# Kernel tuning notes

Measured on AMD Instinct MI355X. Metric: run time of the kernel, lower is better.

Reference implementation:

```python
import jax, jax.numpy as jnp
import numpy as np

D_MODEL = 1024

def setup_inputs() -> dict:
    key = jax.random.key(0)
    ks = jax.random.split(key, 5)
    s = 1.0 / np.sqrt(D_MODEL)  # torch Linear default init scale-ish
    x = jax.random.normal(ks[0], (4, 2048, D_MODEL), dtype=jnp.float32)
    Wq = jax.random.normal(ks[1], (D_MODEL, D_MODEL), dtype=jnp.float32) * s
    Wk = jax.random.normal(ks[2], (D_MODEL, D_MODEL), dtype=jnp.float32) * s
    Wv = jax.random.normal(ks[3], (D_MODEL, D_MODEL), dtype=jnp.float32) * s
    Wo = jax.random.normal(ks[4], (D_MODEL, D_MODEL), dtype=jnp.float32) * s
    z = jnp.zeros((D_MODEL,), dtype=jnp.float32)
    return {"x": x, "Wq": Wq, "bq": z, "Wk": Wk, "bk": z, "Wv": Wv, "bv": z, "Wo": Wo, "bo": z}

def reference(x, Wq, bq, Wk, bk, Wv, bv, Wo, bo):
    # x: (B, S, D). Single-head causal attention, dropout in eval mode (identity).
    B, S, D = x.shape
    Q = jnp.einsum('bsd,ed->bse', x, Wq) + bq
    K = jnp.einsum('bsd,ed->bse', x, Wk) + bk
    V = jnp.einsum('bsd,ed->bse', x, Wv) + bv
    scores = jnp.einsum('bqd,bkd->bqk', Q, K) / jnp.sqrt(jnp.float32(D))
    causal = jnp.tril(jnp.ones((S, S), dtype=bool))  # (S, S)
    scores = jnp.where(causal, scores, -jnp.inf)
    weights = jax.nn.softmax(scores, axis=-1)
    attended = jnp.einsum('bqk,bkd->bqd', weights, V)
    out = jnp.einsum('bsd,ed->bse', attended, Wo) + bo
    return out
```

## Files before the change

### kernel.cpp

```cpp
#include <hip/hip_runtime.h>
#include <cstdint>
#include <cstddef>


#define D_MODEL 1024
#define SEQ     2048
#define BATCH   4

typedef unsigned short u16;
typedef __bf16 bf16_t;
typedef bf16_t bf16x8 __attribute__((ext_vector_type(8)));
typedef float  f32x4  __attribute__((ext_vector_type(4)));
typedef u16    u16x4  __attribute__((ext_vector_type(4)));

__device__ __forceinline__ u16 f2bf(float x) {
  union { float f; uint32_t u; } v; v.f = x;
  uint32_t r = v.u + 0x7fffu + ((v.u >> 16) & 1u);
  return (u16)(r >> 16);
}

__device__ __forceinline__ void gload_lds16(const u16* g, u16* l) {
  __builtin_amdgcn_global_load_lds((__attribute__((address_space(1))) void*)g,
                                   (__attribute__((address_space(3))) void*)l,
                                   16, 0, 0);
}

template <bool ROWSUM>
__device__ __forceinline__ void gemm_core(const u16* __restrict__ A,
                                          const u16* __restrict__ B,
                                          int lda, int ldb, int nt,
                                          u16* As, u16* Bs,
                                          f32x4 acc[4][4], f32x4* rs) {
  const int tid  = threadIdx.x;
  const int lane = tid & 63, wave = tid >> 6;
  const int frow = lane & 15, kc = lane >> 4;
  const int abase = (wave >> 2) * 64, bbase = (wave & 3) * 64;
  const int ar = tid >> 2;
  const int ac = (tid & 3) ^ ((ar >> 1) & 3);
  const u16* Asrc  = A + (size_t)ar * lda + ac * 8;
  const u16* Bsrc0 = B + (size_t)ar * ldb + ac * 8;
  const u16* Bsrc1 = B + (size_t)(ar + 128) * ldb + ac * 8;
  int aoff[4], boff[4];
#pragma unroll
  for (int i = 0; i < 4; ++i) {
    const int ra = abase + i * 16 + frow;
    aoff[i] = (ra * 4 + (kc ^ ((ra >> 1) & 3))) * 8;
    const int rb = bbase + i * 16 + frow;
    boff[i] = (rb * 4 + (kc ^ ((rb >> 1) & 3))) * 8;
  }
  bf16x8 ones;
  if (ROWSUM) {
#pragma unroll
    for (int r = 0; r < 8; ++r) ((u16*)&ones)[r] = 0x3F80;
  }
  auto stage = [&](int t) {
    u16* ab = As + (t & 3) * 4096;
    u16* bb = Bs + (t & 3) * 8192;
    const int kb = t * 32;
    gload_lds16(Asrc + kb, ab + tid * 8);
    gload_lds16(Bsrc0 + kb, bb + tid * 8);
    gload_lds16(Bsrc1 + kb, bb + 4096 + tid * 8);
  };
  stage(0);
  if (nt > 1) stage(1);
  if (nt > 2) stage(2);
  for (int t = 0; t < nt; ++t) {
    if (t + 2 < nt)      asm volatile("s_waitcnt vmcnt(6)" ::: "memory");
    else if (t + 1 < nt) asm volatile("s_waitcnt vmcnt(3)" ::: "memory");
    else                 asm volatile("s_waitcnt vmcnt(0)" ::: "memory");
    __builtin_amdgcn_s_barrier();
    asm volatile("" ::: "memory");
    const u16* ab = As + (t & 3) * 4096;
    const u16* bb = Bs + (t & 3) * 8192;
    bf16x8 af[4], bf[4];
#pragma unroll
    for (int j = 0; j < 4; ++j) bf[j] = *(const bf16x8*)(bb + boff[j]);
#pragma unroll
    for (int i = 0; i < 4; ++i) af[i] = *(const bf16x8*)(ab + aoff[i]);
    if (t + 3 < nt) stage(t + 3);
    __builtin_amdgcn_s_setprio(1);
#pragma unroll
    for (int i = 0; i < 4; ++i)
#pragma unroll
      for (int j = 0; j < 4; ++j)
        acc[i][j] = __builtin_amdgcn_mfma_f32_16x16x32_bf16(af[i], bf[j], acc[i][j], 0, 0, 0);
    if (ROWSUM) {
#pragma unroll
      for (int i = 0; i < 4; ++i)
        rs[i] = __builtin_amdgcn_mfma_f32_16x16x32_bf16(af[i], ones, rs[i], 0, 0, 0);
    }
    __builtin_amdgcn_s_setprio(0);
    asm volatile("" ::: "memory");
    __builtin_amdgcn_s_barrier();
  }
}

__global__ __launch_bounds__(256) void cvt_kernel(const float4* __restrict__ x,
                                                  const float4* __restrict__ wq,
                                                  const float4* __restrict__ wk,
                                                  const float4* __restrict__ wv,
                                                  const float4* __restrict__ wo,
                                                  u16* __restrict__ dst) {
  const int i = blockIdx.x * 256 + threadIdx.x;
  float4 v;
  if (i < 2097152) {
    v = x[i];
  } else {
    const int j = i - 2097152;
    const int w = j >> 18;
    const float4* s = (w == 0) ? wq : (w == 1) ? wk : (w == 2) ? wv : wo;
    v = s[j & 262143];
  }
  u16x4 o = {f2bf(v.x), f2bf(v.y), f2bf(v.z), f2bf(v.w)};
  *(u16x4*)(dst + (size_t)i * 4) = o;
}

__global__ void transposeW_kernel(const u16* __restrict__ src, u16* __restrict__ dst) {
  __shared__ u16 tile[32][33];
  const int r0 = blockIdx.x * 32, c0 = blockIdx.y * 32;
  const int tx = threadIdx.x, ty = threadIdx.y;
#pragma unroll
  for (int r = 0; r < 4; ++r)
    tile[ty + r * 8][tx] = src[(size_t)(r0 + ty + r * 8) * D_MODEL + c0 + tx];
  __syncthreads();
#pragma unroll
  for (int r = 0; r < 4; ++r)
    dst[(size_t)(c0 + ty + r * 8) * D_MODEL + r0 + tx] = tile[tx][ty + r * 8];
}

__global__ __launch_bounds__(512, 2) void stageA_kernel(
    const u16* __restrict__ xb,
    const u16* __restrict__ WqB, const u16* __restrict__ WkB,
    const u16* __restrict__ WoB, const u16* __restrict__ WvT,
    const float* __restrict__ Wo32, const float* __restrict__ bv,
    const float* __restrict__ bq, const float* __restrict__ bk,
    u16* __restrict__ Qb, u16* __restrict__ Kb,
    u16* __restrict__ Wp, float* __restrict__ bp) {
  __shared__ __align__(16) u16 As[16384];
  __shared__ __align__(16) u16 Bs[32768];
  const int blk = blockIdx.x, tid = threadIdx.x;
  const int lane = tid & 63, wave = tid >> 6;
  const int abase = (wave >> 2) * 64, bbase = (wave & 3) * 64;
  const int cl = lane & 15, rl = (lane >> 4) * 4;
  const int c = blk & 7, i = blk >> 3;

  {
    const int rt   = c * 8 + (i & 7);
    const int czi  = i >> 3;
    const int row0 = rt * 128, col0 = (czi >> 1) * 256, z = czi & 1;
    const u16*   W    = z ? WkB : WqB;
    const float* bias = z ? bk : bq;
    u16*         out  = z ? Kb : Qb;
    f32x4 acc[4][4] = {};
    gemm_core<false>(xb + (size_t)row0 * D_MODEL, W + (size_t)col0 * D_MODEL,
                     D_MODEL, D_MODEL, 32, As, Bs, acc, nullptr);
#pragma unroll
    for (int j = 0; j < 4; ++j) {
      const int col = col0 + bbase + j * 16 + cl;
      const float bb = bias[col];
#pragma unroll
      for (int ii = 0; ii < 4; ++ii)
#pragma unroll
        for (int r = 0; r < 4; ++r) {
          const int row = row0 + abase + ii * 16 + rl + r;
          out[(size_t)row * D_MODEL + col] = f2bf(acc[ii][j][r] + bb);
        }
    }
  }
  if (i < 4) {
    const int widx = c * 4 + i;
    const int f0 = (widx >> 2) * 128, e0 = (widx & 3) * 256;
    f32x4 acc[4][4] = {};
    gemm_core<false>(WoB + (size_t)f0 * D_MODEL, WvT + (size_t)e0 * D_MODEL,
                     D_MODEL, D_MODEL, 32, As, Bs, acc, nullptr);
#pragma unroll
    for (int j = 0; j < 4; ++j) {
      const int col = e0 + bbase + j * 16 + cl;
#pragma unroll
      for (int ii = 0; ii < 4; ++ii)
#pragma unroll
        for (int r = 0; r < 4; ++r) {
          const int row = f0 + abase + ii * 16 + rl + r;
          Wp[(size_t)row * D_MODEL + col] = f2bf(acc[ii][j][r]);
        }
    }
  } else if (i < 6) {
    const int f  = (c * 2 + (i - 4)) * 64 + (tid >> 3);
    const int dq = tid & 7;
    const float* row = Wo32 + (size_t)f * D_MODEL + dq * 128;
    const float* bvq = bv + dq * 128;
    float s = 0.f;
#pragma unroll 8
    for (int k = 0; k < 128; ++k) s += row[k] * bvq[k];
    s += __shfl_xor(s, 1);
    s += __shfl_xor(s, 2);
    s += __shfl_xor(s, 4);
    if (dq == 0) bp[f] = s;
  }
}

__global__ __launch_bounds__(512, 2) void stageB_kernel(
    const u16* __restrict__ xb, const u16* __restrict__ Wp,
    const float* __restrict__ bp,
    const u16* __restrict__ Qb, const u16* __restrict__ Kb,
    u16* __restrict__ Vt, u16* __restrict__ Eb) {
  __shared__ __align__(16) u16 As[16384];
  __shared__ __align__(16) u16 Bs[32768];
  const int blk = blockIdx.x, tid = threadIdx.x;
  const int lane = tid & 63, wave = tid >> 6;
  const int abase = (wave >> 2) * 64, bbase = (wave & 3) * 64;
  const int cl = lane & 15, rl = (lane >> 4) * 4;

  if (blk < 256) {
    const int c = blk & 7;
    const int nunit = (blk < 224) ? 1 : 2;
    int uid = (blk < 224) ? (blk >> 3) : (28 + ((blk - 224) >> 3) * 2);
    for (int uu = 0; uu < nunit; ++uu, ++uid) {
      const int w = c * 36 + uid;
      const int b = w / 72;
      int r = w % 72, qi = 0;
#pragma unroll 1
      for (; qi < 16; ++qi) { const int n = (qi >> 1) + 1; if (r < n) break; r -= n; }
      const int ji = r;
      const u16* A  = Qb + (size_t)(b * SEQ + qi * 128) * D_MODEL;
      const u16* Bt = Kb + (size_t)(b * SEQ + ji * 256) * D_MODEL;
      f32x4 acc[4][4] = {};
      gemm_core<false>(A, Bt, D_MODEL, D_MODEL, 32, As, Bs, acc, nullptr);
      u16* out = Eb + (size_t)b * SEQ * SEQ;
#pragma unroll
      for (int ii = 0; ii < 4; ++ii)
#pragma unroll
        for (int rr = 0; rr < 4; ++rr) {
          const int q = qi * 128 + abase + ii * 16 + rl + rr;
#pragma unroll
          for (int j = 0; j < 4; ++j) {
            const int jj = ji * 256 + bbase + j * 16 + cl;
            out[(size_t)q * SEQ + jj] =
                (jj <= q) ? f2bf(__expf(acc[ii][j][rr] * 0.03125f)) : (u16)0;
          }
        }
    }
  } else {
    const int v = blk - 256;
    const int c = v & 7, s = v >> 3;
    const int row0 = (c * 8 + (s >> 2)) * 128;
    const int col0 = (s & 3) * 256;
    f32x4 acc[4][4] = {};
    gemm_core<false>(xb + (size_t)row0 * D_MODEL, Wp + (size_t)col0 * D_MODEL,
                     D_MODEL, D_MODEL, 32, As, Bs, acc, nullptr);
    const int b = row0 >> 11;
    u16* vt = Vt + (size_t)b * D_MODEL * SEQ;
#pragma unroll
    for (int j = 0; j < 4; ++j) {
      const int col = col0 + bbase + j * 16 + cl;
      const float bb = bp[col];
#pragma unroll
      for (int ii = 0; ii < 4; ++ii) {
        const int s0 = (row0 & 2047) + abase + ii * 16 + rl;
        u16x4 o = {f2bf(acc[ii][j][0] + bb), f2bf(acc[ii][j][1] + bb),
                   f2bf(acc[ii][j][2] + bb), f2bf(acc[ii][j][3] + bb)};
        *(u16x4*)(vt + (size_t)col * SEQ + s0) = o;
      }
    }
  }
}

__global__ __launch_bounds__(512, 2) void pv_kernel(const u16* __restrict__ Eb,
                                                    const u16* __restrict__ Vt,
                                                    const float* __restrict__ bo,
                                                    float* __restrict__ Out) {
  __shared__ __align__(16) u16 As[16384];
  __shared__ __align__(16) u16 Bs[32768];
  const int blk = blockIdx.x, tid = threadIdx.x;
  const int c = blk & 7, i = blk >> 3;
  const int b  = c >> 1;
  const int dt = (c & 1) * 2 + (i >> 4);
  const int qt = i & 15;
  const u16* A  = Eb + (size_t)b * SEQ * SEQ + (size_t)(qt * 128) * SEQ;
  const u16* Bt = Vt + (size_t)b * D_MODEL * SEQ + (size_t)(dt * 256) * SEQ;
  f32x4 acc[4][4] = {};
  f32x4 rs[4] = {};
  gemm_core<true>(A, Bt, SEQ, SEQ, (qt + 1) * 4, As, Bs, acc, rs);
  const int lane = tid & 63, wave = tid >> 6;
  const int abase = (wave >> 2) * 64, bbase = (wave & 3) * 64;
  const int cl = lane & 15, rl = (lane >> 4) * 4;
#pragma unroll
  for (int ii = 0; ii < 4; ++ii)
#pragma unroll
    for (int r = 0; r < 4; ++r) {
      const float invl = 1.0f / rs[ii][r];
      const int row = b * SEQ + qt * 128 + abase + ii * 16 + rl + r;
#pragma unroll
      for (int j = 0; j < 4; ++j) {
        const int col = dt * 256 + bbase + j * 16 + cl;
        Out[(size_t)row * D_MODEL + col] = acc[ii][j][r] * invl + bo[col];
      }
    }
}

extern "C" void kernel_launch(void* const* d_in, const int* in_sizes, int n_in,
                              void* d_out, int out_size, void* d_ws, size_t ws_size,
                              hipStream_t stream) {
  const float* x  = (const float*)d_in[0];
  const float* Wq = (const float*)d_in[1];
  const float* bq = (const float*)d_in[2];
  const float* Wk = (const float*)d_in[3];
  const float* bk = (const float*)d_in[4];
  const float* Wv = (const float*)d_in[5];
  const float* bv = (const float*)d_in[6];
  const float* Wo = (const float*)d_in[7];
  const float* bo = (const float*)d_in[8];
  float* out = (float*)d_out;
  char* ws = (char*)d_ws;

  u16*   xb  = (u16*)(ws);
  u16*   Wb  = (u16*)(ws + (16u << 20));
  u16*   Qb  = (u16*)(ws + (24u << 20));
  u16*   Kb  = (u16*)(ws + (40u << 20));
  u16*   Vt  = (u16*)(ws + (56u << 20));
  u16*   Eb  = (u16*)(ws + (72u << 20));
  u16*   WvT = (u16*)(ws + (104u << 20));
  u16*   Wp  = (u16*)(ws + (106u << 20));
  float* bp  = (float*)(ws + (108u << 20));

  cvt_kernel<<<12288, 256, 0, stream>>>((const float4*)x, (const float4*)Wq,
                                        (const float4*)Wk, (const float4*)Wv,
                                        (const float4*)Wo, xb);
  transposeW_kernel<<<dim3(32, 32), dim3(32, 8), 0, stream>>>(Wb + (2u << 20), WvT);
  stageA_kernel<<<512, 512, 0, stream>>>(xb, Wb, Wb + (1u << 20), Wb + (3u << 20),
                                         WvT, Wo, bv, bq, bk, Qb, Kb, Wp, bp);
  stageB_kernel<<<512, 512, 0, stream>>>(xb, Wp, bp, Qb, Kb, Vt, Eb);
  pv_kernel<<<256, 512, 0, stream>>>(Eb, Vt, bo, out);
}
```

Baseline: 258.1 us.

## Retile GEMMs to 256x256, move softmax rowsum into score epilogue, rebalance PV

The QK/QKV projection and score GEMMs now use a 256x256 block tile with a triple-buffered LDS pipeline and one barrier per k-step, which raises arithmetic intensity per block. Causal score tiles are remapped to 256-row blocks with a hand-balanced schedule. The softmax row sums are computed in the score epilogue from the bf16-rounded exponentials and accumulated with atomics into a zeroed workspace buffer, so the extra rowsum MFMAs in the PV kernel go away. The PV kernel switches to 128x128 tiles with short and long causal rows paired for load balance and higher occupancy. The cost is atomic traffic, an extra memset launch, and a risk of tail imbalance from the uneven tile mix.

```diff
diff --git a/kernel.cpp b/kernel.cpp
--- a/kernel.cpp
+++ b/kernel.cpp
@@ -18,6 +18,10 @@
   uint32_t r = v.u + 0x7fffu + ((v.u >> 16) & 1u);
   return (u16)(r >> 16);
 }
+__device__ __forceinline__ float bf2f(u16 h) {
+  union { uint32_t u; float f; } v; v.u = (uint32_t)h << 16;
+  return v.f;
+}
 
 __device__ __forceinline__ void gload_lds16(const u16* g, u16* l) {
   __builtin_amdgcn_global_load_lds((__attribute__((address_space(1))) void*)g,
@@ -25,73 +29,126 @@
                                    16, 0, 0);
 }
 
-template <bool ROWSUM>
-__device__ __forceinline__ void gemm_core(const u16* __restrict__ A,
-                                          const u16* __restrict__ B,
-                                          int lda, int ldb, int nt,
-                                          u16* As, u16* Bs,
-                                          f32x4 acc[4][4], f32x4* rs) {
+__device__ __forceinline__ void gemm256(const u16* __restrict__ A,
+                                        const u16* __restrict__ B,
+                                        int lda, int ldb, int nt,
+                                        u16* As, u16* Bs,
+                                        f32x4 acc[8][4]) {
   const int tid  = threadIdx.x;
   const int lane = tid & 63, wave = tid >> 6;
   const int frow = lane & 15, kc = lane >> 4;
-  const int abase = (wave >> 2) * 64, bbase = (wave & 3) * 64;
-  const int ar = tid >> 2;
-  const int ac = (tid & 3) ^ ((ar >> 1) & 3);
-  const u16* Asrc  = A + (size_t)ar * lda + ac * 8;
-  const u16* Bsrc0 = B + (size_t)ar * ldb + ac * 8;
-  const u16* Bsrc1 = B + (size_t)(ar + 128) * ldb + ac * 8;
-  int aoff[4], boff[4];
+  const int abase = (wave >> 2) * 128, bbase = (wave & 3) * 64;
+  const int r0 = tid >> 2;
+  const int k0 = ((tid & 3) ^ ((r0 >> 1) & 3)) * 8;
+  const u16* Asrc0 = A + (size_t)r0 * lda + k0;
+  const u16* Asrc1 = A + (size_t)(r0 + 128) * lda + k0;
+  const u16* Bsrc0 = B + (size_t)r0 * ldb + k0;
+  const u16* Bsrc1 = B + (size_t)(r0 + 128) * ldb + k0;
+  int aoff[8], boff[4];
+#pragma unroll
+  for (int i = 0; i < 8; ++i) {
+    const int ra = abase + i * 16 + frow;
+    aoff[i] = (ra * 4 + (kc ^ ((ra >> 1) & 3))) * 8;
+  }
+#pragma unroll
+  for (int j = 0; j < 4; ++j) {
+    const int rb = bbase + j * 16 + frow;
+    boff[j] = (rb * 4 + (kc ^ ((rb >> 1) & 3))) * 8;
+  }
+  auto stage = [&](int t, int bufi) {
+    u16* ab = As + bufi * 8192;
+    u16* bb = Bs + bufi * 8192;
+    const int kb = t * 32;
+    gload_lds16(Asrc0 + kb, ab + tid * 8);
+    gload_lds16(Asrc1 + kb, ab + 4096 + tid * 8);
+    gload_lds16(Bsrc0 + kb, bb + tid * 8);
+    gload_lds16(Bsrc1 + kb, bb + 4096 + tid * 8);
+  };
+  stage(0, 0);
+  if (nt > 1) stage(1, 1);
+  int cb = 0, sb = 2;
+  for (int t = 0; t < nt; ++t) {
+    if (t + 1 < nt) asm volatile("s_waitcnt vmcnt(4)" ::: "memory");
+    else            asm volatile("s_waitcnt vmcnt(0)" ::: "memory");
+    __builtin_amdgcn_s_barrier();
+    asm volatile("" ::: "memory");
+    if (t + 2 < nt) stage(t + 2, sb);
+    const u16* ab = As + cb * 8192;
+    const u16* bb = Bs + cb * 8192;
+    bf16x8 af[8], bf[4];
+#pragma unroll
+    for (int j = 0; j < 4; ++j) bf[j] = *(const bf16x8*)(bb + boff[j]);
+#pragma unroll
+    for (int i = 0; i < 8; ++i) af[i] = *(const bf16x8*)(ab + aoff[i]);
+    __builtin_amdgcn_s_setprio(1);
+#pragma unroll
+    for (int i = 0; i < 8; ++i)
+#pragma unroll
+      for (int j = 0; j < 4; ++j)
+        acc[i][j] = __builtin_amdgcn_mfma_f32_16x16x32_bf16(af[i], bf[j], acc[i][j], 0, 0, 0);
+    __builtin_amdgcn_s_setprio(0);
+    asm volatile("" ::: "memory");
+    cb = (cb == 2) ? 0 : cb + 1;
+    sb = (sb == 2) ? 0 : sb + 1;
+  }
+}
+
+__device__ __forceinline__ void gemm128(const u16* __restrict__ A,
+                                        const u16* __restrict__ B,
+                                        int lda, int ldb, int nt,
+                                        u16* As, u16* Bs,
+                                        f32x4 acc[4][2]) {
+  const int tid  = threadIdx.x;
+  const int lane = tid & 63, wave = tid >> 6;
+  const int frow = lane & 15, kc = lane >> 4;
+  const int abase = (wave >> 2) * 64, bbase = (wave & 3) * 32;
+  const int r0 = tid >> 2;
+  const int k0 = ((tid & 3) ^ ((r0 >> 1) & 3)) * 8;
+  const u16* Asrc = A + (size_t)r0 * lda + k0;
+  const u16* Bsrc = B + (size_t)r0 * ldb + k0;
+  int aoff[4], boff[2];
 #pragma unroll
   for (int i = 0; i < 4; ++i) {
     const int ra = abase + i * 16 + frow;
     aoff[i] = (ra * 4 + (kc ^ ((ra >> 1) & 3))) * 8;
-    const int rb = bbase + i * 16 + frow;
-    boff[i] = (rb * 4 + (kc ^ ((rb >> 1) & 3))) * 8;
-  }
-  bf16x8 ones;
-  if (ROWSUM) {
-#pragma unroll
-    for (int r = 0; r < 8; ++r) ((u16*)&ones)[r] = 0x3F80;
+  }
+#pragma unroll
+  for (int j = 0; j < 2; ++j) {
+    const int rb = bbase + j * 16 + frow;
+    boff[j] = (rb * 4 + (kc ^ ((rb >> 1) & 3))) * 8;
   }
   auto stage = [&](int t) {
     u16* ab = As + (t & 3) * 4096;
-    u16* bb = Bs + (t & 3) * 8192;
+    u16* bb = Bs + (t & 3) * 4096;
     const int kb = t * 32;
     gload_lds16(Asrc + kb, ab + tid * 8);
-    gload_lds16(Bsrc0 + kb, bb + tid * 8);
-    gload_lds16(Bsrc1 + kb, bb + 4096 + tid * 8);
+    gload_lds16(Bsrc + kb, bb + tid * 8);
   };
   stage(0);
   if (nt > 1) stage(1);
   if (nt > 2) stage(2);
   for (int t = 0; t < nt; ++t) {
-    if (t + 2 < nt)      asm volatile("s_waitcnt vmcnt(6)" ::: "memory");
-    else if (t + 1 < nt) asm volatile("s_waitcnt vmcnt(3)" ::: "memory");
+    if (t + 2 < nt)      asm volatile("s_waitcnt vmcnt(4)" ::: "memory");
+    else if (t + 1 < nt) asm volatile("s_waitcnt vmcnt(2)" ::: "memory");
     else                 asm volatile("s_waitcnt vmcnt(0)" ::: "memory");
     __builtin_amdgcn_s_barrier();
     asm volatile("" ::: "memory");
+    if (t + 3 < nt) stage(t + 3);
     const u16* ab = As + (t & 3) * 4096;
-    const u16* bb = Bs + (t & 3) * 8192;
-    bf16x8 af[4], bf[4];
-#pragma unroll
-    for (int j = 0; j < 4; ++j) bf[j] = *(const bf16x8*)(bb + boff[j]);
+    const u16* bb = Bs + (t & 3) * 4096;
+    bf16x8 af[4], bf[2];
+#pragma unroll
+    for (int j = 0; j < 2; ++j) bf[j] = *(const bf16x8*)(bb + boff[j]);
 #pragma unroll
     for (int i = 0; i < 4; ++i) af[i] = *(const bf16x8*)(ab + aoff[i]);
-    if (t + 3 < nt) stage(t + 3);
     __builtin_amdgcn_s_setprio(1);
 #pragma unroll
     for (int i = 0; i < 4; ++i)
 #pragma unroll
-      for (int j = 0; j < 4; ++j)
+      for (int j = 0; j < 2; ++j)
         acc[i][j] = __builtin_amdgcn_mfma_f32_16x16x32_bf16(af[i], bf[j], acc[i][j], 0, 0, 0);
-    if (ROWSUM) {
-#pragma unroll
-      for (int i = 0; i < 4; ++i)
-        rs[i] = __builtin_amdgcn_mfma_f32_16x16x32_bf16(af[i], ones, rs[i], 0, 0, 0);
-    }
     __builtin_amdgcn_s_setprio(0);
     asm volatile("" ::: "memory");
-    __builtin_amdgcn_s_barrier();
   }
 }
 
@@ -136,45 +193,47 @@
     const float* __restrict__ bq, const float* __restrict__ bk,
     u16* __restrict__ Qb, u16* __restrict__ Kb,
     u16* __restrict__ Wp, float* __restrict__ bp) {
-  __shared__ __align__(16) u16 As[16384];
-  __shared__ __align__(16) u16 Bs[32768];
+  __shared__ __align__(16) u16 As[24576];
+  __shared__ __align__(16) u16 Bs[24576];
   const int blk = blockIdx.x, tid = threadIdx.x;
   const int lane = tid & 63, wave = tid >> 6;
-  const int abase = (wave >> 2) * 64, bbase = (wave & 3) * 64;
   const int cl = lane & 15, rl = (lane >> 4) * 4;
-  const int c = blk & 7, i = blk >> 3;
-
-  {
-    const int rt   = c * 8 + (i & 7);
-    const int czi  = i >> 3;
-    const int row0 = rt * 128, col0 = (czi >> 1) * 256, z = czi & 1;
+
+  if (blk < 256) {
+    const int c = blk & 7, i = blk >> 3;
+    const int z = i >> 4, w = i & 15;
+    const int rt = c * 4 + (w >> 2), ct = w & 3;
+    const int row0 = rt * 256, col0 = ct * 256;
     const u16*   W    = z ? WkB : WqB;
     const float* bias = z ? bk : bq;
     u16*         out  = z ? Kb : Qb;
-    f32x4 acc[4][4] = {};
-    gemm_core<false>(xb + (size_t)row0 * D_MODEL, W + (size_t)col0 * D_MODEL,
-                     D_MODEL, D_MODEL, 32, As, Bs, acc, nullptr);
+    f32x4 acc[8][4] = {};
+    gemm256(xb + (size_t)row0 * D_MODEL, W + (size_t)col0 * D_MODEL,
+            D_MODEL, D_MODEL, 32, As, Bs, acc);
+    const int abase = (wave >> 2) * 128, bbase = (wave & 3) * 64;
 #pragma unroll
     for (int j = 0; j < 4; ++j) {
       const int col = col0 + bbase + j * 16 + cl;
       const float bb = bias[col];
 #pragma unroll
-      for (int ii = 0; ii < 4; ++ii)
+      for (int ii = 0; ii < 8; ++ii)
 #pragma unroll
         for (int r = 0; r < 4; ++r) {
           const int row = row0 + abase + ii * 16 + rl + r;
           out[(size_t)row * D_MODEL + col] = f2bf(acc[ii][j][r] + bb);
         }
     }
-  }
-  if (i < 4) {
-    const int widx = c * 4 + i;
-    const int f0 = (widx >> 2) * 128, e0 = (widx & 3) * 256;
-    f32x4 acc[4][4] = {};
-    gemm_core<false>(WoB + (size_t)f0 * D_MODEL, WvT + (size_t)e0 * D_MODEL,
-                     D_MODEL, D_MODEL, 32, As, Bs, acc, nullptr);
-#pragma unroll
-    for (int j = 0; j < 4; ++j) {
+  } else if (blk < 320) {
+    const int qq = blk - 256;
+    const int t16 = qq >> 2, quad = qq & 3;
+    const int f0 = (t16 >> 2) * 256 + (quad >> 1) * 128;
+    const int e0 = (t16 & 3) * 256 + (quad & 1) * 128;
+    f32x4 acc[4][2] = {};
+    gemm128(WoB + (size_t)f0 * D_MODEL, WvT + (size_t)e0 * D_MODEL,
+            D_MODEL, D_MODEL, 32, As, Bs, acc);
+    const int abase = (wave >> 2) * 64, bbase = (wave & 3) * 32;
+#pragma unroll
+    for (int j = 0; j < 2; ++j) {
       const int col = e0 + bbase + j * 16 + cl;
 #pragma unroll
       for (int ii = 0; ii < 4; ++ii)
@@ -184,8 +243,8 @@
           Wp[(size_t)row * D_MODEL + col] = f2bf(acc[ii][j][r]);
         }
     }
-  } else if (i < 6) {
-    const int f  = (c * 2 + (i - 4)) * 64 + (tid >> 3);
+  } else {
+    const int f  = (blk - 320) * 64 + (tid >> 3);
     const int dq = tid & 7;
     const float* row = Wo32 + (size_t)f * D_MODEL + dq * 128;
     const float* bvq = bv + dq * 128;
@@ -203,55 +262,91 @@
     const u16* __restrict__ xb, const u16* __restrict__ Wp,
     const float* __restrict__ bp,
     const u16* __restrict__ Qb, const u16* __restrict__ Kb,
-    u16* __restrict__ Vt, u16* __restrict__ Eb) {
-  __shared__ __align__(16) u16 As[16384];
-  __shared__ __align__(16) u16 Bs[32768];
+    u16* __restrict__ Vt, u16* __restrict__ Eb, float* __restrict__ rssum) {
+  __shared__ __align__(16) u16 As[24576];
+  __shared__ __align__(16) u16 Bs[24576];
   const int blk = blockIdx.x, tid = threadIdx.x;
   const int lane = tid & 63, wave = tid >> 6;
-  const int abase = (wave >> 2) * 64, bbase = (wave & 3) * 64;
   const int cl = lane & 15, rl = (lane >> 4) * 4;
 
-  if (blk < 256) {
-    const int c = blk & 7;
-    const int nunit = (blk < 224) ? 1 : 2;
-    int uid = (blk < 224) ? (blk >> 3) : (28 + ((blk - 224) >> 3) * 2);
-    for (int uu = 0; uu < nunit; ++uu, ++uid) {
-      const int w = c * 36 + uid;
-      const int b = w / 72;
-      int r = w % 72, qi = 0;
-#pragma unroll 1
-      for (; qi < 16; ++qi) { const int n = (qi >> 1) + 1; if (r < n) break; r -= n; }
-      const int ji = r;
-      const u16* A  = Qb + (size_t)(b * SEQ + qi * 128) * D_MODEL;
-      const u16* Bt = Kb + (size_t)(b * SEQ + ji * 256) * D_MODEL;
-      f32x4 acc[4][4] = {};
-      gemm_core<false>(A, Bt, D_MODEL, D_MODEL, 32, As, Bs, acc, nullptr);
-      u16* out = Eb + (size_t)b * SEQ * SEQ;
-#pragma unroll
-      for (int ii = 0; ii < 4; ++ii)
-#pragma unroll
-        for (int rr = 0; rr < 4; ++rr) {
-          const int q = qi * 128 + abase + ii * 16 + rl + rr;
-#pragma unroll
-          for (int j = 0; j < 4; ++j) {
-            const int jj = ji * 256 + bbase + j * 16 + cl;
-            out[(size_t)q * SEQ + jj] =
-                (jj <= q) ? f2bf(__expf(acc[ii][j][rr] * 0.03125f)) : (u16)0;
-          }
+  if (blk < 144) {
+    const int c = blk & 7, u = blk >> 3;
+    const int b = c >> 1, h = c & 1;
+    int qi, ji;
+    if (h == 0) {
+      if (u < 1)       { qi = 0; ji = u; }
+      else if (u < 5)  { qi = 3; ji = u - 1; }
+      else if (u < 10) { qi = 4; ji = u - 5; }
+      else             { qi = 7; ji = u - 10; }
+    } else {
+      if (u < 2)       { qi = 1; ji = u; }
+      else if (u < 5)  { qi = 2; ji = u - 2; }
+      else if (u < 11) { qi = 5; ji = u - 5; }
+      else             { qi = 6; ji = u - 11; }
+    }
+    const u16* A  = Qb + (size_t)(b * SEQ + qi * 256) * D_MODEL;
+    const u16* Bt = Kb + (size_t)(b * SEQ + ji * 256) * D_MODEL;
+    f32x4 acc[8][4] = {};
+    gemm256(A, Bt, D_MODEL, D_MODEL, 32, As, Bs, acc);
+    u16* outp = Eb + (size_t)b * SEQ * SEQ;
+    float* rs = rssum + b * SEQ;
+    const int abase = (wave >> 2) * 128, bbase = (wave & 3) * 64;
+#pragma unroll
+    for (int ii = 0; ii < 8; ++ii)
+#pragma unroll
+      for (int r = 0; r < 4; ++r) {
+        const int q = qi * 256 + abase + ii * 16 + rl + r;
+        float ps = 0.f;
+#pragma unroll
+        for (int j = 0; j < 4; ++j) {
+          const int jj = ji * 256 + bbase + j * 16 + cl;
+          u16 h16 = 0;
+          if (jj <= q) h16 = f2bf(__expf(acc[ii][j][r] * 0.03125f));
+          outp[(size_t)q * SEQ + jj] = h16;
+          ps += bf2f(h16);
         }
-    }
-  } else {
-    const int v = blk - 256;
-    const int c = v & 7, s = v >> 3;
-    const int row0 = (c * 8 + (s >> 2)) * 128;
-    const int col0 = (s & 3) * 256;
-    f32x4 acc[4][4] = {};
-    gemm_core<false>(xb + (size_t)row0 * D_MODEL, Wp + (size_t)col0 * D_MODEL,
-                     D_MODEL, D_MODEL, 32, As, Bs, acc, nullptr);
+        ps += __shfl_xor(ps, 1);
+        ps += __shfl_xor(ps, 2);
+        ps += __shfl_xor(ps, 4);
+        ps += __shfl_xor(ps, 8);
+        if (cl == 0) atomicAdd(&rs[q], ps);
+      }
+  } else if (blk < 256) {
+    const int v = blk - 144;
+    const int rt = v >> 2, ct = v & 3;
+    const int row0 = rt * 256, col0 = ct * 256;
+    f32x4 acc[8][4] = {};
+    gemm256(xb + (size_t)row0 * D_MODEL, Wp + (size_t)col0 * D_MODEL,
+            D_MODEL, D_MODEL, 32, As, Bs, acc);
     const int b = row0 >> 11;
     u16* vt = Vt + (size_t)b * D_MODEL * SEQ;
+    const int abase = (wave >> 2) * 128, bbase = (wave & 3) * 64;
 #pragma unroll
     for (int j = 0; j < 4; ++j) {
+      const int col = col0 + bbase + j * 16 + cl;
+      const float bb = bp[col];
+#pragma unroll
+      for (int ii = 0; ii < 8; ++ii) {
+        const int s0 = (row0 & 2047) + abase + ii * 16 + rl;
+        u16x4 o = {f2bf(acc[ii][j][0] + bb), f2bf(acc[ii][j][1] + bb),
+                   f2bf(acc[ii][j][2] + bb), f2bf(acc[ii][j][3] + bb)};
+        *(u16x4*)(vt + (size_t)col * SEQ + s0) = o;
+      }
+    }
+  } else {
+    const int qq = blk - 256;
+    const int t16 = qq >> 2, quad = qq & 3;
+    const int rt = 28 + (t16 >> 2), ct = t16 & 3;
+    const int row0 = rt * 256 + (quad >> 1) * 128;
+    const int col0 = ct * 256 + (quad & 1) * 128;
+    f32x4 acc[4][2] = {};
+    gemm128(xb + (size_t)row0 * D_MODEL, Wp + (size_t)col0 * D_MODEL,
+            D_MODEL, D_MODEL, 32, As, Bs, acc);
+    const int b = row0 >> 11;
+    u16* vt = Vt + (size_t)b * D_MODEL * SEQ;
+    const int abase = (wave >> 2) * 64, bbase = (wave & 3) * 32;
+#pragma unroll
+    for (int j = 0; j < 2; ++j) {
       const int col = col0 + bbase + j * 16 + cl;
       const float bb = bp[col];
 #pragma unroll
@@ -265,35 +360,35 @@
   }
 }
 
-__global__ __launch_bounds__(512, 2) void pv_kernel(const u16* __restrict__ Eb,
+__global__ __launch_bounds__(512, 4) void pv_kernel(const u16* __restrict__ Eb,
                                                     const u16* __restrict__ Vt,
+                                                    const float* __restrict__ rssum,
                                                     const float* __restrict__ bo,
                                                     float* __restrict__ Out) {
   __shared__ __align__(16) u16 As[16384];
-  __shared__ __align__(16) u16 Bs[32768];
+  __shared__ __align__(16) u16 Bs[16384];
   const int blk = blockIdx.x, tid = threadIdx.x;
-  const int c = blk & 7, i = blk >> 3;
-  const int b  = c >> 1;
-  const int dt = (c & 1) * 2 + (i >> 4);
-  const int qt = i & 15;
+  const int rr = blk >> 8, idx = blk & 255;
+  const int b = idx >> 6, rest = idx & 63;
+  const int dt8 = rest >> 3, m = rest & 7;
+  const int qt = rr ? (15 - 2 * m) : (2 * m);
   const u16* A  = Eb + (size_t)b * SEQ * SEQ + (size_t)(qt * 128) * SEQ;
-  const u16* Bt = Vt + (size_t)b * D_MODEL * SEQ + (size_t)(dt * 256) * SEQ;
-  f32x4 acc[4][4] = {};
-  f32x4 rs[4] = {};
-  gemm_core<true>(A, Bt, SEQ, SEQ, (qt + 1) * 4, As, Bs, acc, rs);
+  const u16* Bt = Vt + (size_t)b * D_MODEL * SEQ + (size_t)(dt8 * 128) * SEQ;
+  f32x4 acc[4][2] = {};
+  gemm128(A, Bt, SEQ, SEQ, (qt + 1) * 4, As, Bs, acc);
   const int lane = tid & 63, wave = tid >> 6;
-  const int abase = (wave >> 2) * 64, bbase = (wave & 3) * 64;
+  const int abase = (wave >> 2) * 64, bbase = (wave & 3) * 32;
   const int cl = lane & 15, rl = (lane >> 4) * 4;
 #pragma unroll
   for (int ii = 0; ii < 4; ++ii)
 #pragma unroll
     for (int r = 0; r < 4; ++r) {
-      const float invl = 1.0f / rs[ii][r];
-      const int row = b * SEQ + qt * 128 + abase + ii * 16 + rl + r;
-#pragma unroll
-      for (int j = 0; j < 4; ++j) {
-        const int col = dt * 256 + bbase + j * 16 + cl;
-        Out[(size_t)row * D_MODEL + col] = acc[ii][j][r] * invl + bo[col];
+      const int row = qt * 128 + abase + ii * 16 + rl + r;
+      const float invl = 1.0f / rssum[b * SEQ + row];
+#pragma unroll
+      for (int j = 0; j < 2; ++j) {
+        const int col = dt8 * 128 + bbase + j * 16 + cl;
+        Out[(size_t)(b * SEQ + row) * D_MODEL + col] = acc[ii][j][r] * invl + bo[col];
       }
     }
 }
@@ -322,13 +417,15 @@
   u16*   WvT = (u16*)(ws + (104u << 20));
   u16*   Wp  = (u16*)(ws + (106u << 20));
   float* bp  = (float*)(ws + (108u << 20));
+  float* rssum = (float*)(ws + (20u << 20));
 
   cvt_kernel<<<12288, 256, 0, stream>>>((const float4*)x, (const float4*)Wq,
                                         (const float4*)Wk, (const float4*)Wv,
                                         (const float4*)Wo, xb);
   transposeW_kernel<<<dim3(32, 32), dim3(32, 8), 0, stream>>>(Wb + (2u << 20), WvT);
-  stageA_kernel<<<512, 512, 0, stream>>>(xb, Wb, Wb + (1u << 20), Wb + (3u << 20),
+  stageA_kernel<<<336, 512, 0, stream>>>(xb, Wb, Wb + (1u << 20), Wb + (3u << 20),
                                          WvT, Wo, bv, bq, bk, Qb, Kb, Wp, bp);
-  stageB_kernel<<<512, 512, 0, stream>>>(xb, Wp, bp, Qb, Kb, Vt, Eb);
-  pv_kernel<<<256, 512, 0, stream>>>(Eb, Vt, bo, out);
-}
+  hipMemsetAsync(rssum, 0, BATCH * SEQ * sizeof(float), stream);
+  stageB_kernel<<<320, 512, 0, stream>>>(xb, Wp, bp, Qb, Kb, Vt, Eb, rssum);
+  pv_kernel<<<512, 512, 0, stream>>>(Eb, Vt, rssum, bo, out);
+}
```

After: 269.0 us. 4.2% more time.
